# Kernel tuning notes

Hardware: AMD Instinct MI355X
Metric: run time of the kernel (lower is better)

## Reference

```python
import jax, jax.numpy as jnp
import numpy as np

N_ATOMS = 50000
N_EDGES = 800000
N_ATOM_BASIS = 128
N_FILTERS = 128
N_GAUSS = 64
CUTOFF = 5.0


def shifted_softplus(x):
    return jax.nn.softplus(x) - jnp.log(2.0)


def setup_inputs() -> dict:
    key = jax.random.key(0)
    ks = jax.random.split(key, 9)
    r = jax.random.normal(ks[0], (N_ATOMS, N_ATOM_BASIS), dtype=jnp.float32)
    # per-edge distances in [0, cutoff)
    e = jax.random.uniform(ks[1], (N_EDGES, 1), dtype=jnp.float32) * CUTOFF
    a = jax.random.randint(ks[2], (N_EDGES, 2), 0, N_ATOMS)  # [dst, src] per edge
    Wf2 = jax.random.normal(ks[3], (N_GAUSS, N_FILTERS), dtype=jnp.float32) / np.sqrt(N_GAUSS)
    bf2 = jnp.zeros((N_FILTERS,), jnp.float32)
    Wa = jax.random.normal(ks[4], (N_ATOM_BASIS, N_FILTERS), dtype=jnp.float32) / np.sqrt(N_ATOM_BASIS)
    W1 = jax.random.normal(ks[5], (N_FILTERS, N_ATOM_BASIS), dtype=jnp.float32) / np.sqrt(N_FILTERS)
    b1 = jnp.zeros((N_ATOM_BASIS,), jnp.float32)
    W2 = jax.random.normal(ks[6], (N_ATOM_BASIS, N_ATOM_BASIS), dtype=jnp.float32) / np.sqrt(N_ATOM_BASIS)
    b2 = jnp.zeros((N_ATOM_BASIS,), jnp.float32)
    return {"r": r, "e": e, "Wf2": Wf2, "bf2": bf2, "Wa": Wa,
            "W1": W1, "b1": b1, "W2": W2, "b2": b2, "a": a}


def reference(r, e, Wf2, bf2, Wa, W1, b1, W2, b2, a):
    # Gaussian smearing of per-edge distances: [E,1] -> [E,G]
    offsets = jnp.linspace(0.0, CUTOFF, N_GAUSS, dtype=jnp.float32)
    width = offsets[1] - offsets[0]
    coeff = -0.5 / (width * width)
    g = jnp.exp(coeff * jnp.square(e - offsets[None, :]))  # [E, G]
    # DistanceFilter2 (DistanceFilter1 output is overwritten in the original code)
    W = g @ Wf2 + bf2                      # [E, F] per-edge filter
    rf = r @ Wa                            # [N, F] AtomFilter (no bias)
    y = rf[a[:, 1]] * W                    # gather src nodes, modulate by filter
    y = jax.ops.segment_sum(y, a[:, 0], num_segments=N_ATOMS)  # scatter-add to dst
    y = shifted_softplus(y @ W1 + b1)      # Dense1
    y = y @ W2 + b2                        # Dense2 (no activation)
    return y
```

## Files before the change

kernel.cpp:

```cpp
#include <hip/hip_runtime.h>
#include <hip/hip_bf16.h>
#include <math.h>

#define NA 50000
#define NE 800000
#define WPB 4
#define NTILE 782
#define EGRID 2048
#define NWAVES (EGRID * WPB)
#define SCAT_BLKS 1536
#define RF_BLKS 782
#define TAB_BLKS 256
#define NTAB 16384
#define BCAP 48
#define CSTR 16

typedef float f32x4 __attribute__((ext_vector_type(4)));
typedef __bf16 bf16x8 __attribute__((ext_vector_type(8)));

__device__ __forceinline__ float ssp(float x) {
    float z  = __expf(-fabsf(x));
    float lp = __logf(1.0f + z);
    return fmaxf(x, 0.0f) + lp - 0.69314718f;
}

__device__ __forceinline__ uint32_t pkbf2(float a, float b) {
    union { __bf16 h[2]; uint32_t u; } x;
    x.h[0] = (__bf16)a; x.h[1] = (__bf16)b;
    return x.u;
}

__global__ __launch_bounds__(256) void pack_weights(const float* __restrict__ Wa,
                                                    const float* __restrict__ W1,
                                                    const float* __restrict__ W2,
                                                    const float* __restrict__ Wf2,
                                                    __bf16* __restrict__ pWaH, __bf16* __restrict__ pWaL,
                                                    __bf16* __restrict__ pW1H, __bf16* __restrict__ pW1L,
                                                    __bf16* __restrict__ pW2H, __bf16* __restrict__ pW2L,
                                                    __bf16* __restrict__ pWf,
                                                    int* __restrict__ cursor) {
    const int t = blockIdx.x * 256 + threadIdx.x;
    const int stride = gridDim.x * 256;
    for (int i = t; i < 16384; i += stride) {
        int k = i >> 7, n = i & 127;
        int ks = k >> 5, km = k & 31, lg = km >> 3, j = km & 7;
        int nt = n >> 4, lr = n & 15;
        int fl = ((((ks * 8 + nt) * 4 + lg) * 16 + lr) << 3) + j;
        int sw = n * 128 + (((k >> 3) ^ (n & 15)) << 3) + (k & 7);
        float v; __bf16 h;
        v = Wa[i]; h = (__bf16)v; pWaH[fl] = h; pWaL[fl] = (__bf16)(v - (float)h);
        v = W1[i]; h = (__bf16)v; pW1H[sw] = h; pW1L[sw] = (__bf16)(v - (float)h);
        v = W2[i]; h = (__bf16)v; pW2H[sw] = h; pW2L[sw] = (__bf16)(v - (float)h);
    }
    for (int i = t; i < 8192; i += stride) {
        int k = i >> 7, n = i & 127;
        int ks = k >> 5, km = k & 31, lg = km >> 3, j = km & 7;
        int nt = n >> 4, lr = n & 15;
        int fl = ((((ks * 8 + nt) * 4 + lg) * 16 + lr) << 3) + j;
        pWf[fl] = (__bf16)Wf2[i];
    }
    for (int i = t; i < NA; i += stride) cursor[(size_t)i * CSTR] = i * BCAP;
}

__device__ __forceinline__ void rf_gemm_g(const float* __restrict__ A,
                                          const __bf16* __restrict__ pWh,
                                          const __bf16* __restrict__ pWl,
                                          void* __restrict__ C, int M,
                                          int blk, int gridn) {
    const int tid  = threadIdx.x;
    const int lane = tid & 63, w = tid >> 6;
    const int lrow = lane & 15, lgrp = lane >> 4;

    for (int base = blk * 64; base < M; base += gridn * 64) {
        const int row  = base + w * 16 + lrow;
        const int rowc = row < M ? row : M - 1;

        f32x4 acc[8];
        #pragma unroll
        for (int nt = 0; nt < 8; ++nt) acc[nt] = (f32x4){0.f, 0.f, 0.f, 0.f};

        #pragma unroll
        for (int ks = 0; ks < 4; ++ks) {
            int k0 = ks * 32 + lgrp * 8;
            float4 f0 = *(const float4*)&A[(size_t)rowc * 128 + k0];
            float4 f1 = *(const float4*)&A[(size_t)rowc * 128 + k0 + 4];
            float av[8] = {f0.x, f0.y, f0.z, f0.w, f1.x, f1.y, f1.z, f1.w};
            bf16x8 ah, al;
            #pragma unroll
            for (int j = 0; j < 8; ++j) {
                __bf16 h = (__bf16)av[j];
                ah[j] = h;
                al[j] = (__bf16)(av[j] - (float)h);
            }
            #pragma unroll
            for (int nt = 0; nt < 8; ++nt) {
                const int goff = (((ks << 3) + nt) << 9) + (lane << 3);
                bf16x8 bh = *(const bf16x8*)&pWh[goff];
                bf16x8 bl = *(const bf16x8*)&pWl[goff];
                acc[nt] = __builtin_amdgcn_mfma_f32_16x16x32_bf16(ah, bh, acc[nt], 0, 0, 0);
                acc[nt] = __builtin_amdgcn_mfma_f32_16x16x32_bf16(ah, bl, acc[nt], 0, 0, 0);
                acc[nt] = __builtin_amdgcn_mfma_f32_16x16x32_bf16(al, bh, acc[nt], 0, 0, 0);
            }
        }

        const int orow = base + w * 16 + lgrp * 4;
        #pragma unroll
        for (int r = 0; r < 4; ++r) {
            if (orow + r < M) {
                #pragma unroll
                for (int nt = 0; nt < 8; ++nt) {
                    ((__hip_bfloat16*)C)[(size_t)(orow + r) * 128 + nt * 16 + lrow] =
                        __float2bfloat16(acc[nt][r]);
                }
            }
        }
    }
}

__device__ __forceinline__ void tab_build(const __bf16* __restrict__ pWf,
                                          const float* __restrict__ bf2,
                                          __hip_bfloat16* __restrict__ wtab,
                                          int blk) {
    const int tid  = threadIdx.x;
    const int lane = tid & 63, w = tid >> 6;
    const int lrow = lane & 15, lgrp = lane >> 4;

    float bv[8];
    #pragma unroll
    for (int nt = 0; nt < 8; ++nt) bv[nt] = bf2[nt * 16 + lrow];

    const float coeff = -0.5f * (63.0f / 5.0f) * (63.0f / 5.0f);
    const int row = blk * 64 + w * 16 + lrow;
    const float ev = ((float)row * 4.0f + 1.5f) * (1.0f / 13107.0f);

    bf16x8 ah[2];
    #pragma unroll
    for (int ks = 0; ks < 2; ++ks) {
        #pragma unroll
        for (int j = 0; j < 8; ++j) {
            int k = ks * 32 + lgrp * 8 + j;
            float dd = ev - (5.0f / 63.0f) * (float)k;
            ah[ks][j] = (__bf16)__expf(coeff * dd * dd);
        }
    }

    f32x4 c[8];
    #pragma unroll
    for (int nt = 0; nt < 8; ++nt) c[nt] = (f32x4){0.f, 0.f, 0.f, 0.f};
    #pragma unroll
    for (int ks = 0; ks < 2; ++ks) {
        #pragma unroll
        for (int nt = 0; nt < 8; ++nt) {
            bf16x8 bh = *(const bf16x8*)&pWf[(((ks << 3) + nt) << 9) + (lane << 3)];
            c[nt] = __builtin_amdgcn_mfma_f32_16x16x32_bf16(ah[ks], bh, c[nt], 0, 0, 0);
        }
    }

    const int orow = blk * 64 + w * 16 + lgrp * 4;
    #pragma unroll
    for (int r = 0; r < 4; ++r) {
        #pragma unroll
        for (int nt = 0; nt < 8; ++nt) {
            wtab[(size_t)(orow + r) * 128 + nt * 16 + lrow] =
                __float2bfloat16(c[nt][r] + bv[nt]);
        }
    }
}

__global__ __launch_bounds__(256) void front_fused(const int* __restrict__ a,
                                                   const float* __restrict__ e,
                                                   int* __restrict__ cursor,
                                                   uint32_t* __restrict__ bucket,
                                                   const float* __restrict__ r,
                                                   const __bf16* __restrict__ pWaH,
                                                   const __bf16* __restrict__ pWaL,
                                                   void* __restrict__ rfb,
                                                   const __bf16* __restrict__ pWf,
                                                   const float* __restrict__ bf2,
                                                   __hip_bfloat16* __restrict__ wtab) {
    if (blockIdx.x < SCAT_BLKS) {
        for (int i = blockIdx.x * 256 + threadIdx.x; i < NE; i += SCAT_BLKS * 256) {
            int2 dp = ((const int2*)a)[i];
            int pos = atomicAdd(&cursor[(size_t)dp.x * CSTR], 1);
            uint32_t eq = (uint32_t)(e[i] * 13107.0f + 0.5f);
            if (pos < dp.x * BCAP + BCAP)
                bucket[pos] = (eq << 16) | (uint32_t)dp.y;
        }
    } else if (blockIdx.x < SCAT_BLKS + RF_BLKS) {
        rf_gemm_g(r, pWaH, pWaL, rfb, NA, blockIdx.x - SCAT_BLKS, RF_BLKS);
    } else {
        tab_build(pWf, bf2, wtab, blockIdx.x - SCAT_BLKS - RF_BLKS);
    }
}

__global__ __launch_bounds__(256, 8) void edge_fused(const int* __restrict__ cursor,
                                                     const uint32_t* __restrict__ bucket,
                                                     const uint32_t* __restrict__ wtab,
                                                     const uint32_t* __restrict__ rfb,
                                                     uint32_t* __restrict__ segb) {
    __shared__ uint32_t su[WPB][BCAP];
    __shared__ int      scnt[WPB][8];

    const int tid  = threadIdx.x;
    const int lane = tid & 63, w = tid >> 6;

    const int wi      = blockIdx.x * WPB + w;
    const int d_start = (int)(((long long)wi * NA) / NWAVES);
    const int d_end   = (int)(((long long)(wi + 1) * NA) / NWAVES);
    const int dcount  = d_end - d_start;

    if (lane < dcount) {
        int c = cursor[(size_t)(d_start + lane) * CSTR] - (d_start + lane) * BCAP;
        scnt[w][lane] = (c < BCAP) ? c : BCAP;
    }
    __builtin_amdgcn_wave_barrier();

    uint32_t* su_w = su[w];

    for (int di = 0; di < dcount; ++di) {
        const int d   = d_start + di;
        const int cnt = scnt[w][di];

        if (lane < BCAP) su_w[lane] = bucket[(size_t)d * BCAP + lane];
        __builtin_amdgcn_wave_barrier();

        float racc0 = 0.0f, racc1 = 0.0f;
        for (int j0 = 0; j0 < cnt; j0 += 16) {
            uint32_t rw[16], tw[16];
            #pragma unroll
            for (int j = 0; j < 16; ++j) {
                int jj = (j0 + j < cnt) ? (j0 + j) : (cnt - 1);
                uint32_t u = su_w[jj];
                rw[j] = rfb[(size_t)(u & 0xFFFFu) * 64 + lane];
                tw[j] = wtab[(size_t)(u >> 18) * 64 + lane];
            }
            #pragma unroll
            for (int j = 0; j < 16; ++j) {
                if (j0 + j < cnt) {
                    racc0 = fmaf(__uint_as_float(rw[j] << 16),
                                 __uint_as_float(tw[j] << 16), racc0);
                    racc1 = fmaf(__uint_as_float(rw[j] & 0xFFFF0000u),
                                 __uint_as_float(tw[j] & 0xFFFF0000u), racc1);
                }
            }
        }
        segb[(size_t)d * 64 + lane] = pkbf2(racc0, racc1);
        __builtin_amdgcn_wave_barrier();
    }
}

__global__ __launch_bounds__(256) void dense1(const uint32_t* __restrict__ segb,
                                              const __bf16* __restrict__ pW1H,
                                              const __bf16* __restrict__ pW1L,
                                              const float* __restrict__ b1,
                                              void* __restrict__ y1b) {
    __shared__ __bf16 sWhi[128 * 128];
    __shared__ __bf16 sWlo[128 * 128];
    const int tid = threadIdx.x;
    {
        const uint4* ph = (const uint4*)pW1H;
        const uint4* pl = (const uint4*)pW1L;
        uint4* dh = (uint4*)sWhi;
        uint4* dl = (uint4*)sWlo;
        for (int i = tid; i < 2048; i += 256) { dh[i] = ph[i]; dl[i] = pl[i]; }
    }
    __syncthreads();

    const int lane = tid & 63, w = tid >> 6;
    const int lrow = lane & 15, lgrp = lane >> 4;
    const __bf16* seg = (const __bf16*)segb;

    float bv[8];
    #pragma unroll
    for (int nt = 0; nt < 8; ++nt) bv[nt] = b1[nt * 16 + lrow];

    const int base = blockIdx.x * 64;
    const int row  = base + w * 16 + lrow;
    const int rowc = row < NA ? row : NA - 1;

    f32x4 acc[8];
    #pragma unroll
    for (int nt = 0; nt < 8; ++nt) acc[nt] = (f32x4){0.f, 0.f, 0.f, 0.f};

    #pragma unroll
    for (int ks = 0; ks < 4; ++ks) {
        int k0 = ks * 32 + lgrp * 8;
        bf16x8 ya = *(const bf16x8*)&seg[(size_t)rowc * 128 + k0];
        #pragma unroll
        for (int nt = 0; nt < 8; ++nt) {
            int n = nt * 16 + lrow;
            int addr = n * 128 + (((ks * 4 + lgrp) ^ (n & 15)) << 3);
            bf16x8 bh = *(const bf16x8*)&sWhi[addr];
            bf16x8 bl = *(const bf16x8*)&sWlo[addr];
            acc[nt] = __builtin_amdgcn_mfma_f32_16x16x32_bf16(ya, bh, acc[nt], 0, 0, 0);
            acc[nt] = __builtin_amdgcn_mfma_f32_16x16x32_bf16(ya, bl, acc[nt], 0, 0, 0);
        }
    }

    const int orow = base + w * 16 + lgrp * 4;
    #pragma unroll
    for (int r = 0; r < 4; ++r) {
        if (orow + r < NA) {
            #pragma unroll
            for (int nt = 0; nt < 8; ++nt) {
                float v = ssp(acc[nt][r] + bv[nt]);
                ((__hip_bfloat16*)y1b)[(size_t)(orow + r) * 128 + nt * 16 + lrow] =
                    __float2bfloat16(v);
            }
        }
    }
}

__global__ __launch_bounds__(256) void dense2(const void* __restrict__ y1b,
                                              const __bf16* __restrict__ pW2H,
                                              const __bf16* __restrict__ pW2L,
                                              const float* __restrict__ b2,
                                              float* __restrict__ out) {
    __shared__ __bf16 sWhi[128 * 128];
    __shared__ __bf16 sWlo[128 * 128];
    const int tid = threadIdx.x;
    {
        const uint4* ph = (const uint4*)pW2H;
        const uint4* pl = (const uint4*)pW2L;
        uint4* dh = (uint4*)sWhi;
        uint4* dl = (uint4*)sWlo;
        for (int i = tid; i < 2048; i += 256) { dh[i] = ph[i]; dl[i] = pl[i]; }
    }
    __syncthreads();

    const int lane = tid & 63, w = tid >> 6;
    const int lrow = lane & 15, lgrp = lane >> 4;
    const __bf16* y1 = (const __bf16*)y1b;

    float bv[8];
    #pragma unroll
    for (int nt = 0; nt < 8; ++nt) bv[nt] = b2[nt * 16 + lrow];

    const int base = blockIdx.x * 64;
    const int row  = base + w * 16 + lrow;
    const int rowc = row < NA ? row : NA - 1;

    f32x4 acc[8];
    #pragma unroll
    for (int nt = 0; nt < 8; ++nt) acc[nt] = (f32x4){0.f, 0.f, 0.f, 0.f};

    #pragma unroll
    for (int ks = 0; ks < 4; ++ks) {
        int k0 = ks * 32 + lgrp * 8;
        bf16x8 ya = *(const bf16x8*)&y1[(size_t)rowc * 128 + k0];
        #pragma unroll
        for (int nt = 0; nt < 8; ++nt) {
            int n = nt * 16 + lrow;
            int addr = n * 128 + (((ks * 4 + lgrp) ^ (n & 15)) << 3);
            bf16x8 bh = *(const bf16x8*)&sWhi[addr];
            bf16x8 bl = *(const bf16x8*)&sWlo[addr];
            acc[nt] = __builtin_amdgcn_mfma_f32_16x16x32_bf16(ya, bh, acc[nt], 0, 0, 0);
            acc[nt] = __builtin_amdgcn_mfma_f32_16x16x32_bf16(ya, bl, acc[nt], 0, 0, 0);
        }
    }

    const int orow = base + w * 16 + lgrp * 4;
    #pragma unroll
    for (int r = 0; r < 4; ++r) {
        if (orow + r < NA) {
            #pragma unroll
            for (int nt = 0; nt < 8; ++nt) {
                out[(size_t)(orow + r) * 128 + nt * 16 + lrow] = acc[nt][r] + bv[nt];
            }
        }
    }
}

extern "C" void kernel_launch(void* const* d_in, const int* in_sizes, int n_in,
                              void* d_out, int out_size, void* d_ws, size_t ws_size,
                              hipStream_t stream) {
    const float* r   = (const float*)d_in[0];
    const float* e   = (const float*)d_in[1];
    const float* Wf2 = (const float*)d_in[2];
    const float* bf2 = (const float*)d_in[3];
    const float* Wa  = (const float*)d_in[4];
    const float* W1  = (const float*)d_in[5];
    const float* b1  = (const float*)d_in[6];
    const float* W2  = (const float*)d_in[7];
    const float* b2  = (const float*)d_in[8];
    const int*   a   = (const int*)d_in[9];

    float* out = (float*)d_out;

    uint32_t* rfb    = (uint32_t*)d_ws;
    uint32_t* segb   = (uint32_t*)d_ws + 3200000;
    uint32_t* bucket = (uint32_t*)d_ws + 6400000;
    __hip_bfloat16* wtab = (__hip_bfloat16*)((uint32_t*)d_ws + 8800000);
    uint32_t* y1b    = (uint32_t*)d_ws + 6400000;
    int*      cursor = (int*)d_ws + 9850000;
    __bf16*   pWaH   = (__bf16*)((int*)d_ws + 10653000);
    __bf16*   pWaL   = pWaH + 16384;
    __bf16*   pW1H   = pWaL + 16384;
    __bf16*   pW1L   = pW1H + 16384;
    __bf16*   pW2H   = pW1L + 16384;
    __bf16*   pW2L   = pW2H + 16384;
    __bf16*   pWf    = pW2L + 16384;

    pack_weights<<<64, 256, 0, stream>>>(Wa, W1, W2, Wf2,
                                         pWaH, pWaL, pW1H, pW1L, pW2H, pW2L,
                                         pWf, cursor);

    front_fused<<<SCAT_BLKS + RF_BLKS + TAB_BLKS, 256, 0, stream>>>(
        a, e, cursor, bucket, r, pWaH, pWaL, rfb, pWf, bf2, wtab);

    edge_fused<<<EGRID, 256, 0, stream>>>(cursor, bucket, (const uint32_t*)wtab,
                                          rfb, segb);

    dense1<<<NTILE, 256, 0, stream>>>(segb, pW1H, pW1L, b1, y1b);
    dense2<<<NTILE, 256, 0, stream>>>(y1b, pW2H, pW2L, b2, out);
}
```

Measured before the change: 154.1 us.

## Replace per-destination atomic bucketing with two-level coarse bin then LDS scatter

The edge scatter now appends 64-bit records into coarse cells, one per group of 128 destinations and per sub-slot keyed by block, using far fewer global atomic counters. A new binscat kernel then reads each coarse bin and distributes the records into per-destination buckets using shared-memory atomics, writing plain counts. This is meant to cut global atomic contention and scattered 4-byte writes in the front kernel. The cost is an extra kernel launch and a second pass over the edge records, plus a fixed sub-cell capacity of 384 that could drop edges if a cell overflows.

```diff
diff --git a/kernel.cpp b/kernel.cpp
--- a/kernel.cpp
+++ b/kernel.cpp
@@ -13,7 +13,10 @@
 #define TAB_BLKS 256
 #define NTAB 16384
 #define BCAP 48
-#define CSTR 16
+#define NBIN 391
+#define NSUB 8
+#define SUBCAP 384
+#define CPAD 16
 
 typedef float f32x4 __attribute__((ext_vector_type(4)));
 typedef __bf16 bf16x8 __attribute__((ext_vector_type(8)));
@@ -38,7 +41,7 @@
                                                     __bf16* __restrict__ pW1H, __bf16* __restrict__ pW1L,
                                                     __bf16* __restrict__ pW2H, __bf16* __restrict__ pW2L,
                                                     __bf16* __restrict__ pWf,
-                                                    int* __restrict__ cursor) {
+                                                    int* __restrict__ ccur) {
     const int t = blockIdx.x * 256 + threadIdx.x;
     const int stride = gridDim.x * 256;
     for (int i = t; i < 16384; i += stride) {
@@ -59,7 +62,7 @@
         int fl = ((((ks * 8 + nt) * 4 + lg) * 16 + lr) << 3) + j;
         pWf[fl] = (__bf16)Wf2[i];
     }
-    for (int i = t; i < NA; i += stride) cursor[(size_t)i * CSTR] = i * BCAP;
+    for (int i = t; i < NBIN * NSUB; i += stride) ccur[i * CPAD] = 0;
 }
 
 __device__ __forceinline__ void rf_gemm_g(const float* __restrict__ A,
@@ -169,8 +172,8 @@
 
 __global__ __launch_bounds__(256) void front_fused(const int* __restrict__ a,
                                                    const float* __restrict__ e,
-                                                   int* __restrict__ cursor,
-                                                   uint32_t* __restrict__ bucket,
+                                                   int* __restrict__ ccur,
+                                                   unsigned long long* __restrict__ coarse,
                                                    const float* __restrict__ r,
                                                    const __bf16* __restrict__ pWaH,
                                                    const __bf16* __restrict__ pWaL,
@@ -179,17 +182,55 @@
                                                    const float* __restrict__ bf2,
                                                    __hip_bfloat16* __restrict__ wtab) {
     if (blockIdx.x < SCAT_BLKS) {
+        const int sub = blockIdx.x & (NSUB - 1);
         for (int i = blockIdx.x * 256 + threadIdx.x; i < NE; i += SCAT_BLKS * 256) {
             int2 dp = ((const int2*)a)[i];
-            int pos = atomicAdd(&cursor[(size_t)dp.x * CSTR], 1);
+            int cell = ((dp.x >> 7) << 3) | sub;
+            int pos = atomicAdd(&ccur[cell * CPAD], 1);
             uint32_t eq = (uint32_t)(e[i] * 13107.0f + 0.5f);
-            if (pos < dp.x * BCAP + BCAP)
-                bucket[pos] = (eq << 16) | (uint32_t)dp.y;
+            if (pos < SUBCAP)
+                coarse[(size_t)cell * SUBCAP + pos] =
+                    ((unsigned long long)(uint32_t)dp.x << 32) |
+                    ((unsigned long long)eq << 16) | (uint32_t)dp.y;
         }
     } else if (blockIdx.x < SCAT_BLKS + RF_BLKS) {
         rf_gemm_g(r, pWaH, pWaL, rfb, NA, blockIdx.x - SCAT_BLKS, RF_BLKS);
     } else {
-        tab_build(pWf, bf2, wtab, blockIdx.x - SCAT_BLKS - RF_BLKS);
+        tab_build(pWf, bf2, wtab, blockIdx.x - SCAT_BLKS - TAB_BLKS >= 0 ?
+                  blockIdx.x - SCAT_BLKS - RF_BLKS : blockIdx.x - SCAT_BLKS - RF_BLKS);
+    }
+}
+
+__global__ __launch_bounds__(256) void binscat(const unsigned long long* __restrict__ coarse,
+                                               const int* __restrict__ ccur,
+                                               uint32_t* __restrict__ bucket,
+                                               int* __restrict__ cursor) {
+    __shared__ int lcur[128];
+    const int bin = blockIdx.x;
+    const int tid = threadIdx.x;
+    if (tid < 128) lcur[tid] = 0;
+    __syncthreads();
+
+    #pragma unroll
+    for (int s = 0; s < NSUB; ++s) {
+        const int cell = (bin << 3) | s;
+        int cb = ccur[cell * CPAD];
+        if (cb > SUBCAP) cb = SUBCAP;
+        for (int i = tid; i < cb; i += 256) {
+            unsigned long long u = coarse[(size_t)cell * SUBCAP + i];
+            int dst = (int)(u >> 32);
+            int pos = atomicAdd(&lcur[dst & 127], 1);
+            if (pos < BCAP)
+                bucket[(size_t)dst * BCAP + pos] = (uint32_t)u;
+        }
+    }
+    __syncthreads();
+    if (tid < 128) {
+        int d = (bin << 7) + tid;
+        if (d < NA) {
+            int c = lcur[tid];
+            cursor[d] = (c < BCAP) ? c : BCAP;
+        }
     }
 }
 
@@ -210,7 +251,7 @@
     const int dcount  = d_end - d_start;
 
     if (lane < dcount) {
-        int c = cursor[(size_t)(d_start + lane) * CSTR] - (d_start + lane) * BCAP;
+        int c = cursor[d_start + lane];
         scnt[w][lane] = (c < BCAP) ? c : BCAP;
     }
     __builtin_amdgcn_wave_barrier();
@@ -389,11 +430,13 @@
 
     uint32_t* rfb    = (uint32_t*)d_ws;
     uint32_t* segb   = (uint32_t*)d_ws + 3200000;
+    unsigned long long* coarse = (unsigned long long*)((uint32_t*)d_ws + 3200000);
     uint32_t* bucket = (uint32_t*)d_ws + 6400000;
     __hip_bfloat16* wtab = (__hip_bfloat16*)((uint32_t*)d_ws + 8800000);
     uint32_t* y1b    = (uint32_t*)d_ws + 6400000;
-    int*      cursor = (int*)d_ws + 9850000;
-    __bf16*   pWaH   = (__bf16*)((int*)d_ws + 10653000);
+    int*      ccur   = (int*)d_ws + 9850000;
+    int*      cursor = (int*)d_ws + 9910000;
+    __bf16*   pWaH   = (__bf16*)((int*)d_ws + 9960000);
     __bf16*   pWaL   = pWaH + 16384;
     __bf16*   pW1H   = pWaL + 16384;
     __bf16*   pW1L   = pW1H + 16384;
@@ -403,10 +446,12 @@
 
     pack_weights<<<64, 256, 0, stream>>>(Wa, W1, W2, Wf2,
                                          pWaH, pWaL, pW1H, pW1L, pW2H, pW2L,
-                                         pWf, cursor);
+                                         pWf, ccur);
 
     front_fused<<<SCAT_BLKS + RF_BLKS + TAB_BLKS, 256, 0, stream>>>(
-        a, e, cursor, bucket, r, pWaH, pWaL, rfb, pWf, bf2, wtab);
+        a, e, ccur, coarse, r, pWaH, pWaL, rfb, pWf, bf2, wtab);
+
+    binscat<<<NBIN, 256, 0, stream>>>(coarse, ccur, bucket, cursor);
 
     edge_fused<<<EGRID, 256, 0, stream>>>(cursor, bucket, (const uint32_t*)wtab,
                                           rfb, segb);
```

Result: faster. 150.4 us (-2.4%).
